# Kernel optimization log

Measured on AMD Instinct MI355X. Metric: run time of the kernel, lower is better.

Reference implementation:

```python
import jax, jax.numpy as jnp
import numpy as np
import math

SIGMA = 0.6  # bandwidths=[0.6]; torch code returns inside the loop so only the first sigma is used
GAMMA = math.gamma((SIGMA + 1.0) / 2.0) / (math.gamma(SIGMA / 2.0) * SIGMA ** 0.5)


def setup_inputs() -> dict:
    key = jax.random.key(0)
    k1, k2 = jax.random.split(key)
    X1 = jax.random.normal(k1, (4096, 128), dtype=jnp.float32)
    X2 = jax.random.normal(k2, (4096, 128), dtype=jnp.float32)
    return {"X1": X1, "X2": X2}


def _student_kernel(G, a_sq, b_sq):
    # G: [a,b] inner products; a_sq/b_sq: squared norms
    d2 = -2.0 * G + a_sq[:, None] + b_sq[None, :]
    return GAMMA * jnp.power(1.0 + d2 / 2.0, -(SIGMA + 1.0) / 2.0)


def _double_center(K):
    # CM @ K @ CM^T  ==  K - rowmean - colmean + totalmean (exact)
    cm = K.mean(axis=0, keepdims=True)  # mean over rows -> subtracted per column
    rm = K.mean(axis=1, keepdims=True)  # mean over cols -> subtracted per row
    tm = K.mean()
    return K - cm - rm + tm


def reference(X1, X2):
    m = X1.shape[0]
    n = X2.shape[0]
    XX = X1 @ X1.T
    XY = X1 @ X2.T
    YY = X2 @ X2.T
    x_sq = jnp.diagonal(XX)
    y_sq = jnp.diagonal(YY)
    K_XX = _student_kernel(XX, x_sq, x_sq)
    K_XY = _student_kernel(XY, x_sq, y_sq)
    K_YY = _student_kernel(YY, y_sq, y_sq)
    C_XX2 = jnp.square(_double_center(K_XX))
    C_XY2 = jnp.square(_double_center(K_XY))
    C_YY2 = jnp.square(_double_center(K_YY))
    # unbiased branch with const_diagonal = sum(wts) = 1 -> trace_X = m, trace_Y = n
    mf = jnp.float32(m)
    nf = jnp.float32(n)
    vdr2 = (jnp.sum(C_XX2) - mf) / ((mf - 1.0) * mf) \
         + (jnp.sum(C_YY2) - nf) / ((nf - 1.0) * nf) \
         - 2.0 * jnp.sum(C_XY2) / (mf * nf)
    return vdr2
```

## Files before the change

kernel.cpp:

```cpp
#include <hip/hip_runtime.h>


typedef __attribute__((ext_vector_type(8))) _Float16 f16x8;
typedef __attribute__((ext_vector_type(4))) float f32x4;

#define LOG2G (-0.99304426f)
#define GAMMA_F 0.50241665f
#define NTILES 8256
#define SLAB (64 * 4096)

#define OFF_SQ1   0
#define OFF_SQ2   16384
#define OFF_H1    32768
#define OFF_H2    1081344
#define OFF_SLABS 2129920
#define OFF_BPART (2129920 + 4194304)
#define OFF_PARTA (OFF_BPART + 33024)

__global__ __launch_bounds__(256) void vdr_prep(const float* __restrict__ X1,
                                                const float* __restrict__ X2,
                                                _Float16* __restrict__ H1,
                                                _Float16* __restrict__ H2,
                                                float* __restrict__ sq1,
                                                float* __restrict__ sq2) {
  const int tid = threadIdx.x;
  const int g = tid & 15;
  const int grow = blockIdx.x * 16 + (tid >> 4);
  const float* X; _Float16* Hf; float* SQ; int row;
  if (grow < 4096) { X = X1; Hf = H1; SQ = sq1; row = grow; }
  else             { X = X2; Hf = H2; SQ = sq2; row = grow - 4096; }
  const float4* src = reinterpret_cast<const float4*>(X + (size_t)row * 128 + g * 8);
  const float4 v0 = src[0];
  const float4 v1 = src[1];
  f16x8 h;
  h[0] = (_Float16)v0.x; h[1] = (_Float16)v0.y; h[2] = (_Float16)v0.z; h[3] = (_Float16)v0.w;
  h[4] = (_Float16)v1.x; h[5] = (_Float16)v1.y; h[6] = (_Float16)v1.z; h[7] = (_Float16)v1.w;
  const int R = row >> 4;
  reinterpret_cast<f16x8*>(Hf)[(size_t)(R * 16 + g) * 16 + (row & 15)] = h;
  float s = v0.x * v0.x + v0.y * v0.y + v0.z * v0.z + v0.w * v0.w
          + v1.x * v1.x + v1.y * v1.y + v1.z * v1.z + v1.w * v1.w;
  #pragma unroll
  for (int o = 1; o < 16; o <<= 1) s += __shfl_xor(s, o);
  if (g == 0) SQ[row] = s;
}

__device__ __forceinline__ void tri_decode(int u, int& bi, int& bj) {
  int b = (int)(64.5f - sqrtf(4160.25f - 2.0f * (float)u));
  if (b < 0) b = 0; if (b > 63) b = 63;
  while (b > 0 && (b * (129 - b)) / 2 > u) --b;
  while (b < 63 && ((b + 1) * (128 - b)) / 2 <= u) ++b;
  bi = b;
  bj = b + (u - (b * (129 - b)) / 2);
}

__global__ __launch_bounds__(256) void vdr_main(const _Float16* __restrict__ H1,
                                                const _Float16* __restrict__ H2,
                                                const float* __restrict__ sq1,
                                                const float* __restrict__ sq2,
                                                float* __restrict__ slabs,
                                                float* __restrict__ bpart) {
  const int w = threadIdx.x >> 6, lane = threadIdx.x & 63;
  const int lr = lane & 15, lg = lane >> 4;
  const int t = blockIdx.x * 4 + w;

  __shared__ float rs_area_s[4][16][65];
  __shared__ float colbuf_s[4][64];
  float (*rs_area)[65] = rs_area_s[w];
  float* colbuf = colbuf_s[w];

  int z, bi, bj; const _Float16 *A, *B; const float *as, *bs;
  if (t < 2080)      { z = 0; tri_decode(t, bi, bj);        A = H1; B = H1; as = sq1; bs = sq1; }
  else if (t < 6176) { z = 1; int v = t - 2080; bi = v >> 6; bj = v & 63;
                                                            A = H1; B = H2; as = sq1; bs = sq2; }
  else               { z = 2; tri_decode(t - 6176, bi, bj); A = H2; B = H2; as = sq2; bs = sq2; }

  f32x4 acc[4][4];
  #pragma unroll
  for (int mi = 0; mi < 4; ++mi)
    #pragma unroll
    for (int ni = 0; ni < 4; ++ni)
      acc[mi][ni] = (f32x4){0.f, 0.f, 0.f, 0.f};

  const f16x8* Af = reinterpret_cast<const f16x8*>(A);
  const f16x8* Bf = reinterpret_cast<const f16x8*>(B);
  #pragma unroll
  for (int ks = 0; ks < 4; ++ks) {
    const int fo = ks * 64 + lane;
    f16x8 a[4], b[4];
    #pragma unroll
    for (int mi = 0; mi < 4; ++mi)
      a[mi] = Af[(size_t)(bi * 4 + mi) * 256 + fo];
    #pragma unroll
    for (int ni = 0; ni < 4; ++ni)
      b[ni] = Bf[(size_t)(bj * 4 + ni) * 256 + fo];
    #pragma unroll
    for (int mi = 0; mi < 4; ++mi)
      #pragma unroll
      for (int ni = 0; ni < 4; ++ni)
        acc[mi][ni] = __builtin_amdgcn_mfma_f32_16x16x32_f16(a[mi], b[ni], acc[mi][ni], 0, 0, 0);
  }

  float cb[4];
  #pragma unroll
  for (int ni = 0; ni < 4; ++ni) cb[ni] = 0.5f * bs[bj * 64 + ni * 16 + lr];
  const bool dg = (z != 1) && (bi == bj);

  float k2s = 0.f;
  float cpart[4] = {0.f, 0.f, 0.f, 0.f};

  #pragma unroll
  for (int mi = 0; mi < 4; ++mi) {
    const float4 aq = *reinterpret_cast<const float4*>(as + bi * 64 + mi * 16 + lg * 4);
    const float aqv[4] = {aq.x, aq.y, aq.z, aq.w};
    #pragma unroll
    for (int rg = 0; rg < 4; ++rg) {
      const float pre = __builtin_fmaf(0.5f, aqv[rg], 1.0f);
      float rp = 0.f;
      #pragma unroll
      for (int ni = 0; ni < 4; ++ni) {
        const float G = acc[mi][ni][rg];
        const float base = (pre + cb[ni]) - G;
        float Kv = __builtin_amdgcn_exp2f(
            __builtin_fmaf(-0.8f, __builtin_amdgcn_logf(base), LOG2G));
        if (dg) { if ((mi * 16 + lg * 4 + rg) == (ni * 16 + lr)) Kv = GAMMA_F; }
        rp += Kv;
        cpart[ni] += Kv;
        k2s = __builtin_fmaf(Kv, Kv, k2s);
      }
      rs_area[lr][mi * 16 + lg * 4 + rg] = rp;
    }
  }

  float rsum = 0.f;
  #pragma unroll
  for (int j = 0; j < 16; ++j) rsum += rs_area[j][lane];

  #pragma unroll
  for (int ni = 0; ni < 4; ++ni) {
    float cp = cpart[ni];
    cp += __shfl_xor(cp, 16);
    cp += __shfl_xor(cp, 32);
    if (lg == 0) colbuf[ni * 16 + lr] = cp;
  }
  const float cval = colbuf[lane];

  float* rowslab = slabs + (size_t)((z == 0) ? 0 : (z == 1) ? 1 : 3) * SLAB;
  rowslab[(size_t)bj * 4096 + bi * 64 + lane] = rsum;
  if (z == 1)
    slabs[(size_t)2 * SLAB + (size_t)bi * 4096 + bj * 64 + lane] = cval;
  else if (bi != bj)
    rowslab[(size_t)bi * 4096 + bj * 64 + lane] = cval;

  #pragma unroll
  for (int o = 32; o; o >>= 1) k2s += __shfl_xor(k2s, o);
  if (lane == 0) {
    const float wt = (z != 1 && bi != bj) ? 2.f : 1.f;
    bpart[t] = wt * k2s;
  }
}

__global__ __launch_bounds__(256) void vdr_reduceA(const float* __restrict__ slabs,
                                                   double* __restrict__ partA) {
  const int j = blockIdx.y, tid = threadIdx.x;
  const int e = blockIdx.x * 256 + tid;
  const float* base = slabs + (size_t)j * SLAB + e;
  double s = 0.0;
  #pragma unroll
  for (int k = 0; k < 64; ++k) s += (double)base[(size_t)k * 4096];
  double sq = s * s, sm = s;
  #pragma unroll
  for (int o = 32; o; o >>= 1) { sq += __shfl_down(sq, o); sm += __shfl_down(sm, o); }
  __shared__ double sh[4][2];
  const int lane = tid & 63, wid = tid >> 6;
  if (lane == 0) { sh[wid][0] = sq; sh[wid][1] = sm; }
  __syncthreads();
  if (tid == 0) {
    partA[(size_t)(j * 16 + blockIdx.x) * 2 + 0] = sh[0][0] + sh[1][0] + sh[2][0] + sh[3][0];
    partA[(size_t)(j * 16 + blockIdx.x) * 2 + 1] = sh[0][1] + sh[1][1] + sh[2][1] + sh[3][1];
  }
}

__global__ __launch_bounds__(256) void vdr_reduceB(const double* __restrict__ partA,
                                                   const float* __restrict__ bpart,
                                                   float* __restrict__ out) {
  const int tid = threadIdx.x;
  __shared__ double ssq[4], ssum[4], s2sh[4][3];
  double s2[3] = {0.0, 0.0, 0.0};
  for (int i = tid; i < NTILES; i += 256) {
    const double v = (double)bpart[i];
    if (i < 2080) s2[0] += v; else if (i < 6176) s2[1] += v; else s2[2] += v;
  }
  #pragma unroll
  for (int o = 32; o; o >>= 1) {
    s2[0] += __shfl_down(s2[0], o);
    s2[1] += __shfl_down(s2[1], o);
    s2[2] += __shfl_down(s2[2], o);
  }
  const int lane = tid & 63, wid = tid >> 6;
  if (lane == 0) { s2sh[wid][0] = s2[0]; s2sh[wid][1] = s2[1]; s2sh[wid][2] = s2[2]; }
  if (tid < 64) {
    const int j = tid >> 4, c = tid & 15;
    double sq = partA[(size_t)(j * 16 + c) * 2 + 0];
    double sm = partA[(size_t)(j * 16 + c) * 2 + 1];
    #pragma unroll
    for (int o = 8; o; o >>= 1) { sq += __shfl_down(sq, o, 16); sm += __shfl_down(sm, o, 16); }
    if (c == 0) { ssq[j] = sq; ssum[j] = sm; }
  }
  __syncthreads();
  if (tid == 0) {
    const double S2XX = s2sh[0][0] + s2sh[1][0] + s2sh[2][0] + s2sh[3][0];
    const double S2XY = s2sh[0][1] + s2sh[1][1] + s2sh[2][1] + s2sh[3][1];
    const double S2YY = s2sh[0][2] + s2sh[1][2] + s2sh[2][2] + s2sh[3][2];
    const double inv = 1.0 / 4096.0;
    const double r0 = S2XX - 2.0 * ssq[0] * inv + ssum[0] * ssum[0] * inv * inv;
    const double r1 = S2XY - ssq[1] * inv - ssq[2] * inv + ssum[1] * ssum[1] * inv * inv;
    const double r2 = S2YY - 2.0 * ssq[3] * inv + ssum[3] * ssum[3] * inv * inv;
    const double mf = 4096.0;
    out[0] = (float)((r0 - mf) / ((mf - 1.0) * mf)
                   + (r2 - mf) / ((mf - 1.0) * mf)
                   - 2.0 * r1 / (mf * mf));
  }
}

extern "C" void kernel_launch(void* const* d_in, const int* in_sizes, int n_in,
                              void* d_out, int out_size, void* d_ws, size_t ws_size,
                              hipStream_t stream) {
  const float* X1 = (const float*)d_in[0];
  const float* X2 = (const float*)d_in[1];
  char* ws = (char*)d_ws;
  float* sq1      = (float*)(ws + OFF_SQ1);
  float* sq2      = (float*)(ws + OFF_SQ2);
  _Float16* H1    = (_Float16*)(ws + OFF_H1);
  _Float16* H2    = (_Float16*)(ws + OFF_H2);
  float* slabs    = (float*)(ws + OFF_SLABS);
  float* bpart    = (float*)(ws + OFF_BPART);
  double* partA   = (double*)(ws + OFF_PARTA);

  vdr_prep<<<512, 256, 0, stream>>>(X1, X2, H1, H2, sq1, sq2);
  vdr_main<<<2064, 256, 0, stream>>>(H1, H2, sq1, sq2, slabs, bpart);
  dim3 ga(16, 4);
  vdr_reduceA<<<ga, 256, 0, stream>>>(slabs, partA);
  vdr_reduceB<<<1, 256, 0, stream>>>(partA, bpart, (float*)d_out);
}
```

Baseline: 50.88 us.

## Use 128x128 block tiles with LDS-shared operand panels across four waves

Each block now computes a 128x128 tile instead of each wave owning an independent 64x64 tile. A and B operands are staged through shared memory so the four waves reuse them, and row and column partial sums are combined across waves before writing to the slabs. This halves the slab size and the reduceA depth, and it cuts global operand loads and partial-sum traffic. In exchange it adds block-wide syncs and LDS staging, and the grid drops to 2080 blocks, which leaves less scheduling granularity on the triangular tiles.

```diff
diff --git a/kernel.cpp b/kernel.cpp
--- a/kernel.cpp
+++ b/kernel.cpp
@@ -6,16 +6,16 @@
 
 #define LOG2G (-0.99304426f)
 #define GAMMA_F 0.50241665f
-#define NTILES 8256
-#define SLAB (64 * 4096)
+#define NT128 2080
+#define SLAB (32 * 4096)
 
 #define OFF_SQ1   0
 #define OFF_SQ2   16384
 #define OFF_H1    32768
 #define OFF_H2    1081344
 #define OFF_SLABS 2129920
-#define OFF_BPART (2129920 + 4194304)
-#define OFF_PARTA (OFF_BPART + 33024)
+#define OFF_BPART 4227072
+#define OFF_PARTA 4235392
 
 __global__ __launch_bounds__(256) void vdr_prep(const float* __restrict__ X1,
                                                 const float* __restrict__ X2,
@@ -44,13 +44,13 @@
   if (g == 0) SQ[row] = s;
 }
 
-__device__ __forceinline__ void tri_decode(int u, int& bi, int& bj) {
-  int b = (int)(64.5f - sqrtf(4160.25f - 2.0f * (float)u));
-  if (b < 0) b = 0; if (b > 63) b = 63;
-  while (b > 0 && (b * (129 - b)) / 2 > u) --b;
-  while (b < 63 && ((b + 1) * (128 - b)) / 2 <= u) ++b;
+__device__ __forceinline__ void tri32(int u, int& bi, int& bj) {
+  int b = (int)(32.5f - sqrtf(1056.25f - 2.0f * (float)u));
+  if (b < 0) b = 0; if (b > 31) b = 31;
+  while (b > 0 && (b * (65 - b)) / 2 > u) --b;
+  while (b < 31 && ((b + 1) * (64 - b)) / 2 <= u) ++b;
   bi = b;
-  bj = b + (u - (b * (129 - b)) / 2);
+  bj = b + (u - (b * (65 - b)) / 2);
 }
 
 __global__ __launch_bounds__(256) void vdr_main(const _Float16* __restrict__ H1,
@@ -59,20 +59,25 @@
                                                 const float* __restrict__ sq2,
                                                 float* __restrict__ slabs,
                                                 float* __restrict__ bpart) {
-  const int w = threadIdx.x >> 6, lane = threadIdx.x & 63;
+  const int tid = threadIdx.x;
+  const int w = tid >> 6, lane = tid & 63;
   const int lr = lane & 15, lg = lane >> 4;
-  const int t = blockIdx.x * 4 + w;
-
-  __shared__ float rs_area_s[4][16][65];
-  __shared__ float colbuf_s[4][64];
-  float (*rs_area)[65] = rs_area_s[w];
-  float* colbuf = colbuf_s[w];
-
-  int z, bi, bj; const _Float16 *A, *B; const float *as, *bs;
-  if (t < 2080)      { z = 0; tri_decode(t, bi, bj);        A = H1; B = H1; as = sq1; bs = sq1; }
-  else if (t < 6176) { z = 1; int v = t - 2080; bi = v >> 6; bj = v & 63;
-                                                            A = H1; B = H2; as = sq1; bs = sq2; }
-  else               { z = 2; tri_decode(t - 6176, bi, bj); A = H2; B = H2; as = sq2; bs = sq2; }
+  const int wr = w >> 1, wc = w & 1;
+
+  __shared__ f16x8 pan[2048];
+  __shared__ float rs_sum[4][64];
+  __shared__ float cs_sum[4][64];
+  __shared__ float sred[4];
+
+  int t = blockIdx.x, z, bi, bj;
+  const _Float16 *A, *B; const float *as, *bs;
+  if (t < 528)       { z = 0; tri32(t, bi, bj);          A = H1; B = H1; as = sq1; bs = sq1; }
+  else if (t < 1552) { z = 1; int v = t - 528; bi = v >> 5; bj = v & 31;
+                                                           A = H1; B = H2; as = sq1; bs = sq2; }
+  else               { z = 2; tri32(t - 1552, bi, bj);    A = H2; B = H2; as = sq2; bs = sq2; }
+
+  const f16x8* Af = reinterpret_cast<const f16x8*>(A);
+  const f16x8* Bf = reinterpret_cast<const f16x8*>(B);
 
   f32x4 acc[4][4];
   #pragma unroll
@@ -81,28 +86,44 @@
     for (int ni = 0; ni < 4; ++ni)
       acc[mi][ni] = (f32x4){0.f, 0.f, 0.f, 0.f};
 
-  const f16x8* Af = reinterpret_cast<const f16x8*>(A);
-  const f16x8* Bf = reinterpret_cast<const f16x8*>(B);
-  #pragma unroll
-  for (int ks = 0; ks < 4; ++ks) {
-    const int fo = ks * 64 + lane;
-    f16x8 a[4], b[4];
-    #pragma unroll
-    for (int mi = 0; mi < 4; ++mi)
-      a[mi] = Af[(size_t)(bi * 4 + mi) * 256 + fo];
-    #pragma unroll
-    for (int ni = 0; ni < 4; ++ni)
-      b[ni] = Bf[(size_t)(bj * 4 + ni) * 256 + fo];
-    #pragma unroll
-    for (int mi = 0; mi < 4; ++mi)
+  #pragma unroll
+  for (int h = 0; h < 2; ++h) {
+    #pragma unroll
+    for (int i = 0; i < 8; ++i) {
+      const int c = w * 8 + i;
+      f16x8 v;
+      if (c < 16)
+        v = Af[(size_t)(bi * 8 + (c >> 1)) * 256 + h * 128 + (c & 1) * 64 + lane];
+      else {
+        const int d = c - 16;
+        v = Bf[(size_t)(bj * 8 + (d >> 1)) * 256 + h * 128 + (d & 1) * 64 + lane];
+      }
+      pan[c * 64 + lane] = v;
+    }
+    __syncthreads();
+    #pragma unroll
+    for (int kk = 0; kk < 2; ++kk) {
+      f16x8 a[4], b[4];
+      #pragma unroll
+      for (int mi = 0; mi < 4; ++mi)
+        a[mi] = pan[(wr * 4 + mi) * 128 + kk * 64 + lane];
       #pragma unroll
       for (int ni = 0; ni < 4; ++ni)
-        acc[mi][ni] = __builtin_amdgcn_mfma_f32_16x16x32_f16(a[mi], b[ni], acc[mi][ni], 0, 0, 0);
-  }
+        b[ni] = pan[1024 + (wc * 4 + ni) * 128 + kk * 64 + lane];
+      #pragma unroll
+      for (int mi = 0; mi < 4; ++mi)
+        #pragma unroll
+        for (int ni = 0; ni < 4; ++ni)
+          acc[mi][ni] = __builtin_amdgcn_mfma_f32_16x16x32_f16(a[mi], b[ni], acc[mi][ni], 0, 0, 0);
+    }
+    __syncthreads();
+  }
+
+  float (*rs_area)[65] = (float (*)[65])((float*)pan + w * 1040);
 
   float cb[4];
   #pragma unroll
-  for (int ni = 0; ni < 4; ++ni) cb[ni] = 0.5f * bs[bj * 64 + ni * 16 + lr];
+  for (int ni = 0; ni < 4; ++ni) cb[ni] = 0.5f * bs[bj * 128 + wc * 64 + ni * 16 + lr];
   const bool dg = (z != 1) && (bi == bj);
 
   float k2s = 0.f;
@@ -110,7 +131,7 @@
 
   #pragma unroll
   for (int mi = 0; mi < 4; ++mi) {
-    const float4 aq = *reinterpret_cast<const float4*>(as + bi * 64 + mi * 16 + lg * 4);
+    const float4 aq = *reinterpret_cast<const float4*>(as + bi * 128 + wr * 64 + mi * 16 + lg * 4);
     const float aqv[4] = {aq.x, aq.y, aq.z, aq.w};
     #pragma unroll
     for (int rg = 0; rg < 4; ++rg) {
@@ -122,7 +143,9 @@
         const float base = (pre + cb[ni]) - G;
         float Kv = __builtin_amdgcn_exp2f(
             __builtin_fmaf(-0.8f, __builtin_amdgcn_logf(base), LOG2G));
-        if (dg) { if ((mi * 16 + lg * 4 + rg) == (ni * 16 + lr)) Kv = GAMMA_F; }
+        if (dg) {
+          if ((wr * 64 + mi * 16 + lg * 4 + rg) == (wc * 64 + ni * 16 + lr)) Kv = GAMMA_F;
+        }
         rp += Kv;
         cpart[ni] += Kv;
         k2s = __builtin_fmaf(Kv, Kv, k2s);
@@ -134,28 +157,37 @@
   float rsum = 0.f;
   #pragma unroll
   for (int j = 0; j < 16; ++j) rsum += rs_area[j][lane];
+  rs_sum[w][lane] = rsum;
 
   #pragma unroll
   for (int ni = 0; ni < 4; ++ni) {
     float cp = cpart[ni];
     cp += __shfl_xor(cp, 16);
     cp += __shfl_xor(cp, 32);
-    if (lg == 0) colbuf[ni * 16 + lr] = cp;
-  }
-  const float cval = colbuf[lane];
+    if (lg == 0) cs_sum[w][ni * 16 + lr] = cp;
+  }
+  #pragma unroll
+  for (int o = 32; o; o >>= 1) k2s += __shfl_xor(k2s, o);
+  if (lane == 0) sred[w] = k2s;
+  __syncthreads();
 
   float* rowslab = slabs + (size_t)((z == 0) ? 0 : (z == 1) ? 1 : 3) * SLAB;
-  rowslab[(size_t)bj * 4096 + bi * 64 + lane] = rsum;
-  if (z == 1)
-    slabs[(size_t)2 * SLAB + (size_t)bi * 4096 + bj * 64 + lane] = cval;
-  else if (bi != bj)
-    rowslab[(size_t)bi * 4096 + bj * 64 + lane] = cval;
-
-  #pragma unroll
-  for (int o = 32; o; o >>= 1) k2s += __shfl_xor(k2s, o);
-  if (lane == 0) {
+  float* colslab = slabs + (size_t)((z == 0) ? 0 : (z == 1) ? 2 : 3) * SLAB;
+  if (tid < 128) {
+    const int r = tid;
+    const float v = rs_sum[(r >> 6) * 2][r & 63] + rs_sum[(r >> 6) * 2 + 1][r & 63];
+    rowslab[(size_t)bj * 4096 + bi * 128 + r] = v;
+  } else {
+    const int c = tid - 128;
+    const float v = cs_sum[c >> 6][c & 63] + cs_sum[(c >> 6) + 2][c & 63];
+    if (z == 1)
+      colslab[(size_t)bi * 4096 + bj * 128 + c] = v;
+    else if (bi != bj)
+      rowslab[(size_t)bi * 4096 + bj * 128 + c] = v;
+  }
+  if (tid == 0) {
     const float wt = (z != 1 && bi != bj) ? 2.f : 1.f;
-    bpart[t] = wt * k2s;
+    bpart[blockIdx.x] = (sred[0] + sred[1] + sred[2] + sred[3]) * wt;
   }
 }
 
@@ -166,7 +198,7 @@
   const float* base = slabs + (size_t)j * SLAB + e;
   double s = 0.0;
   #pragma unroll
-  for (int k = 0; k < 64; ++k) s += (double)base[(size_t)k * 4096];
+  for (int k = 0; k < 32; ++k) s += (double)base[(size_t)k * 4096];
   double sq = s * s, sm = s;
   #pragma unroll
   for (int o = 32; o; o >>= 1) { sq += __shfl_down(sq, o); sm += __shfl_down(sm, o); }
@@ -186,9 +218,9 @@
   const int tid = threadIdx.x;
   __shared__ double ssq[4], ssum[4], s2sh[4][3];
   double s2[3] = {0.0, 0.0, 0.0};
-  for (int i = tid; i < NTILES; i += 256) {
+  for (int i = tid; i < NT128; i += 256) {
     const double v = (double)bpart[i];
-    if (i < 2080) s2[0] += v; else if (i < 6176) s2[1] += v; else s2[2] += v;
+    if (i < 528) s2[0] += v; else if (i < 1552) s2[1] += v; else s2[2] += v;
   }
   #pragma unroll
   for (int o = 32; o; o >>= 1) {
@@ -237,7 +269,7 @@
   double* partA   = (double*)(ws + OFF_PARTA);
 
   vdr_prep<<<512, 256, 0, stream>>>(X1, X2, H1, H2, sq1, sq2);
-  vdr_main<<<2064, 256, 0, stream>>>(H1, H2, sq1, sq2, slabs, bpart);
+  vdr_main<<<NT128, 256, 0, stream>>>(H1, H2, sq1, sq2, slabs, bpart);
   dim3 ga(16, 4);
   vdr_reduceA<<<ga, 256, 0, stream>>>(slabs, partA);
   vdr_reduceB<<<1, 256, 0, stream>>>(partA, bpart, (float*)d_out);
```

New measurement: 54.71 us. 1.08x slower.
